# Optimization experiments

Measured on AMD Instinct MI355X. Metric: run time of the kernel, lower is better.

Reference implementation:

```python
import jax, jax.numpy as jnp
import numpy as np

B, S, D, H, DK, F = 4, 2048, 1024, 16, 64, 4096


def layer_norm(x, g, b, eps=1e-5):
    mu = jnp.mean(x, axis=-1, keepdims=True)
    var = jnp.var(x, axis=-1, keepdims=True)
    return (x - mu) * jax.lax.rsqrt(var + eps) * g + b


def setup_inputs() -> dict:
    key = jax.random.key(0)
    ks = jax.random.split(key, 16)
    s = 0.02
    return {
        "src": jax.random.normal(ks[0], (B, S, D), jnp.float32),
        # per-head q/k/v projections stacked over heads: (H, D, DK)
        "Wq": jax.random.normal(ks[1], (H, D, DK), jnp.float32) * s,
        "bq": jnp.zeros((H, DK), jnp.float32),
        "Wk": jax.random.normal(ks[2], (H, D, DK), jnp.float32) * s,
        "bk": jnp.zeros((H, DK), jnp.float32),
        "Wv": jax.random.normal(ks[3], (H, D, DK), jnp.float32) * s,
        "bv": jnp.zeros((H, DK), jnp.float32),
        "Wo": jax.random.normal(ks[4], (H * DK, D), jnp.float32) * s,
        "bo": jnp.zeros((D,), jnp.float32),
        "ln1_g": jnp.ones((D,), jnp.float32),
        "ln1_b": jnp.zeros((D,), jnp.float32),
        "W1": jax.random.normal(ks[5], (D, F), jnp.float32) * s,
        "b1": jnp.zeros((F,), jnp.float32),
        "W2": jax.random.normal(ks[6], (F, D), jnp.float32) * s,
        "b2": jnp.zeros((D,), jnp.float32),
        "ln2_g": jnp.ones((D,), jnp.float32),
        "ln2_b": jnp.zeros((D,), jnp.float32),
    }


def reference(src, Wq, bq, Wk, bk, Wv, bv, Wo, bo, ln1_g, ln1_b, W1, b1, W2, b2, ln2_g, ln2_b):
    # --- multi-head attention (all heads batched via einsum) ---
    q = jnp.einsum("bsd,hdk->bhsk", src, Wq) + bq[None, :, None, :]
    k = jnp.einsum("bsd,hdk->bhsk", src, Wk) + bk[None, :, None, :]
    v = jnp.einsum("bsd,hdk->bhsk", src, Wv) + bv[None, :, None, :]
    scale = jnp.sqrt(jnp.asarray(DK, q.dtype))
    scores = jnp.einsum("bhqk,bhsk->bhqs", q, k) / scale  # [B,H,S,S]
    p = jax.nn.softmax(scores, axis=-1)
    ctx = jnp.einsum("bhqs,bhsk->bhqk", p, v)             # [B,H,S,DK]
    ctx = ctx.transpose(0, 2, 1, 3).reshape(src.shape[0], src.shape[1], H * DK)
    attn_out = ctx @ Wo + bo
    x = layer_norm(src + attn_out, ln1_g, ln1_b)
    # --- feed-forward ---
    ff = jax.nn.relu(x @ W1 + b1) @ W2 + b2
    return layer_norm(x + ff, ln2_g, ln2_b)
```

## Files before the change

### kernel.cpp

```cpp
#include <hip/hip_runtime.h>
#include <hip/hip_bf16.h>
#include <cstddef>
#include <cstdint>

typedef __bf16 bf16;
typedef __bf16 bf16x4 __attribute__((ext_vector_type(4)));
typedef __bf16 bf16x8 __attribute__((ext_vector_type(8)));
typedef float f32x4 __attribute__((ext_vector_type(4)));
typedef float f32x16 __attribute__((ext_vector_type(16)));
typedef unsigned int u32x4 __attribute__((ext_vector_type(4)));

#define GLD_LDS16(g, l) __builtin_amdgcn_global_load_lds( \
    (const __attribute__((address_space(1))) void*)(g),   \
    (__attribute__((address_space(3))) void*)(l), 16, 0, 0)

#define SBAR __builtin_amdgcn_s_barrier()
#define SCHED0 __builtin_amdgcn_sched_barrier(0)
#define VMW(n) asm volatile("s_waitcnt vmcnt(" #n ")" ::: "memory")

static __device__ inline unsigned int cvtpk(float lo, float hi) {
  unsigned int r;
  asm("v_cvt_pk_bf16_f32 %0, %1, %2" : "=v"(r) : "v"(lo), "v"(hi));
  return r;
}
static __device__ inline void plswap(unsigned int& a, unsigned int& b) {
  asm("v_permlane32_swap_b32 %0, %1" : "+v"(a), "+v"(b));
}
static __device__ inline float fexp2(float x) {
#if __has_builtin(__builtin_amdgcn_exp2f)
  return __builtin_amdgcn_exp2f(x);
#else
  float r; asm("v_exp_f32 %0, %1" : "=v"(r) : "v"(x)); return r;
#endif
}
static __device__ inline float tsum16(const float* e) {
  float s0 = e[0] + e[1], s1 = e[2] + e[3], s2 = e[4] + e[5], s3 = e[6] + e[7];
  float s4 = e[8] + e[9], s5 = e[10] + e[11], s6 = e[12] + e[13], s7 = e[14] + e[15];
  return ((s0 + s1) + (s2 + s3)) + ((s4 + s5) + (s6 + s7));
}

__global__ void __launch_bounds__(256)
k_cast(const float* __restrict__ in, bf16* __restrict__ out) {
  int gid = blockIdx.x * 256 + threadIdx.x;
  f32x4 a = ((const f32x4*)in)[gid * 2];
  f32x4 b = ((const f32x4*)in)[gid * 2 + 1];
  bf16x8 o;
#pragma unroll
  for (int i = 0; i < 4; ++i) { o[i] = (bf16)a[i]; o[i + 4] = (bf16)b[i]; }
  ((bf16x8*)out)[gid] = o;
}

__global__ void __launch_bounds__(256)
k_transpose_t(const float* __restrict__ in, bf16* __restrict__ out, int R, int C) {
  __shared__ float tile[64][68];
  const int nct = C >> 6;
  const int bc = blockIdx.x % nct, br = blockIdx.x / nct;
  const int r0 = br << 6, c0 = bc << 6;
  const int t = threadIdx.x;
  const int tr = t >> 4, tc4 = (t & 15) << 2;
#pragma unroll
  for (int i = 0; i < 4; ++i)
    *(f32x4*)&tile[i * 16 + tr][tc4] =
        *(const f32x4*)&in[(size_t)(r0 + i * 16 + tr) * C + c0 + tc4];
  __syncthreads();
  const int c = t >> 2, rch = (t & 3) << 4;
  bf16 ob[16];
#pragma unroll
  for (int j = 0; j < 16; ++j) ob[j] = (bf16)tile[rch + j][c];
  bf16* dst = out + (size_t)(c0 + c) * R + r0 + rch;
  *(bf16x8*)&dst[0] = *(bf16x8*)&ob[0];
  *(bf16x8*)&dst[8] = *(bf16x8*)&ob[8];
}

__global__ void __launch_bounds__(256)
k_reorder_qkv_t(const float* __restrict__ Wq, const float* __restrict__ Wk,
                const float* __restrict__ Wv, bf16* __restrict__ WqkvT) {
  __shared__ float tile[64][68];
  const int bid = blockIdx.x;
  const int sub = bid >> 4, tl = bid & 15;
  const int proj = sub >> 4, h = sub & 15;
  const float* W = (proj == 0) ? Wq : (proj == 1) ? Wk : Wv;
  const float* src = W + (size_t)h * 65536;
  const int r0 = tl << 6;
  const int t = threadIdx.x, tr = t >> 4, tc4 = (t & 15) << 2;
#pragma unroll
  for (int i = 0; i < 4; ++i)
    *(f32x4*)&tile[i * 16 + tr][tc4] =
        *(const f32x4*)&src[(size_t)(r0 + i * 16 + tr) * 64 + tc4];
  __syncthreads();
  const int c = t >> 2, rch = (t & 3) << 4;
  bf16 ob[16];
#pragma unroll
  for (int j = 0; j < 16; ++j) ob[j] = (bf16)tile[rch + j][c];
  bf16* dst = WqkvT + ((size_t)(proj * 1024 + h * 64 + c)) * 1024 + r0 + rch;
  *(bf16x8*)&dst[0] = *(bf16x8*)&ob[0];
  *(bf16x8*)&dst[8] = *(bf16x8*)&ob[8];
}

__global__ void __launch_bounds__(256)
k_bias_qkv(const float* __restrict__ bq, const float* __restrict__ bk,
           const float* __restrict__ bv, float* __restrict__ bqkv) {
  int n = blockIdx.x * 256 + threadIdx.x;
  int proj = n >> 10, wi = n & 1023;
  const float* bb = (proj == 0) ? bq : (proj == 1) ? bk : bv;
  bqkv[n] = bb[wi];
}

template <int MODE, int NREP>
__global__ void __launch_bounds__(512, 1)
k_gemm4(const bf16* __restrict__ A, const bf16* __restrict__ Bt,
        const float* __restrict__ bias, void* __restrict__ outp,
        int M, int N, int K,
        bf16* __restrict__ qb, bf16* __restrict__ kb, bf16* __restrict__ vb) {
  constexpr int BN = 128 * NREP;
  constexpr int BROWS = 64 * NREP;
  __shared__ __align__(16) bf16 Asl[4][8192];
  __shared__ __align__(16) bf16 Bsl[4][BROWS * 64];

  const int tid = threadIdx.x;
  const int lane = tid & 63, wave = tid >> 6;
  const int l16 = lane & 15, lq = lane >> 4;
  const int qwm = wave >> 2, qwn = wave & 3;

  const int mtiles = M >> 8;
  const int wg = blockIdx.x;
  const int tile_m = (wg % mtiles) << 8;
  const int tile_n = (wg / mtiles) * BN;

  const bf16* Abase = A + (size_t)tile_m * K;
  const bf16* Bbase = Bt + (size_t)tile_n * K;

  const int crow = tid >> 3;
  const int ccol = ((tid & 7) ^ (crow & 7)) << 3;

  auto stageA = [&](int T, int h, int slot) {
    const bf16* s_ = Abase + (size_t)(h * 128 + crow) * K + T * 64 + ccol;
    GLD_LDS16(s_, &Asl[slot][tid * 8]);
    GLD_LDS16(s_ + (size_t)64 * K, &Asl[slot][tid * 8 + 4096]);
  };
  auto stageB = [&](int T, int h, int slot) {
    const bf16* s_ = Bbase + (size_t)(h * BROWS + crow) * K + T * 64 + ccol;
    GLD_LDS16(s_, &Bsl[slot][tid * 8]);
    if (NREP == 2) GLD_LDS16(s_ + (size_t)64 * K, &Bsl[slot][tid * 8 + 4096]);
  };

  const int xk = l16 & 7;
  const int swz0 = (lq ^ xk) * 16;
  const int swz1 = ((4 | lq) ^ xk) * 16;
  const int arow_b = (qwm * 64 + l16) * 128;
  const int brow_b = (qwn * 16 * NREP + l16) * 128;

  bf16x8 af[4][2];
  bf16x8 bb[2][NREP][2];
  f32x4 acc[2][2][4][NREP] = {};

  auto dsA = [&](int slot) {
    const char* Ab = (const char*)&Asl[slot][0] + arow_b;
#pragma unroll
    for (int mi = 0; mi < 4; ++mi) {
      af[mi][0] = *(const bf16x8*)(Ab + mi * 2048 + swz0);
      af[mi][1] = *(const bf16x8*)(Ab + mi * 2048 + swz1);
    }
  };
  auto dsB2 = [&](int slot0, int slot1) {
    const char* B0 = (const char*)&Bsl[slot0][0] + brow_b;
    const char* B1 = (const char*)&Bsl[slot1][0] + brow_b;
#pragma unroll
    for (int ni = 0; ni < NREP; ++ni) {
      bb[0][ni][0] = *(const bf16x8*)(B0 + ni * 2048 + swz0);
      bb[0][ni][1] = *(const bf16x8*)(B0 + ni * 2048 + swz1);
      bb[1][ni][0] = *(const bf16x8*)(B1 + ni * 2048 + swz0);
      bb[1][ni][1] = *(const bf16x8*)(B1 + ni * 2048 + swz1);
    }
  };
  auto MF2 = [&](int mh) {
    __builtin_amdgcn_s_setprio(1);
#pragma unroll
    for (int nh = 0; nh < 2; ++nh)
#pragma unroll
      for (int mi = 0; mi < 4; ++mi)
#pragma unroll
        for (int ni = 0; ni < NREP; ++ni)
#pragma unroll
          for (int p = 0; p < 2; ++p)
            acc[mh][nh][mi][ni] = __builtin_amdgcn_mfma_f32_16x16x32_bf16(
                af[mi][p], bb[nh][ni][p], acc[mh][nh][mi][ni], 0, 0, 0);
    __builtin_amdgcn_s_setprio(0);
  };

  const int NT = K >> 6;
  const int NI = NT >> 1;

  stageA(0, 0, 0); stageA(0, 1, 1); stageB(0, 0, 0); stageB(0, 1, 1);
  stageA(1, 0, 2); stageB(1, 0, 2); stageB(1, 1, 3);
  SCHED0;
  if (NREP == 2) { VMW(6); } else { VMW(4); }
  SBAR;

  for (int i = 0; i < NI; ++i) {
    const int t2 = 2 * i + 2, t3 = 2 * i + 3;
    const bool tv = (t2 < NT);
    dsA(0); dsB2(0, 1);
    stageA(2 * i + 1, 1, 3);
    SCHED0;
    if (NREP == 2) { VMW(10); } else { VMW(7); }
    SBAR; MF2(0); SBAR;
    dsA(1);
    if (tv) { stageA(t2, 0, 0); stageB(t2, 0, 0); }
    SCHED0;
    if (!tv) { VMW(2); }
    else if (NREP == 2) { VMW(6); } else { VMW(5); }
    SBAR; MF2(1); SBAR;
    dsA(2); dsB2(2, 3);
    if (tv) { stageA(t2, 1, 1); stageB(t2, 1, 1); }
    SCHED0;
    if (!tv) { VMW(0); }
    else if (NREP == 2) { VMW(8); } else { VMW(6); }
    SBAR; MF2(0); SBAR;
    dsA(3);
    if (tv) {
      stageA(t3, 0, 2); stageB(t3, 0, 2); stageB(t3, 1, 3);
      SCHED0;
      if (NREP == 2) { VMW(6); } else { VMW(4); }
    }
    SBAR; MF2(1); SBAR;
  }

#pragma unroll
  for (int mh = 0; mh < 2; ++mh)
#pragma unroll
    for (int nh = 0; nh < 2; ++nh)
#pragma unroll
      for (int mi = 0; mi < 4; ++mi)
#pragma unroll
        for (int ni = 0; ni < NREP; ++ni) {
          const int gn = tile_n + nh * (BN / 2) + qwn * 16 * NREP + ni * 16 + l16;
          const float bv = bias[gn];
          f32x4 v = acc[mh][nh][mi][ni];
          const int gm0 = tile_m + mh * 128 + qwm * 64 + mi * 16 + lq * 4;
          if (MODE == 0) {
            int proj = gn >> 10, wi = gn & 1023;
            int h = wi >> 6, dk = wi & 63;
            int b = gm0 >> 11, sdx = gm0 & 2047;
            size_t bhs = (size_t)((b << 4) + h);
            if (proj == 0) {
#pragma unroll
              for (int i2 = 0; i2 < 4; ++i2)
                qb[(bhs * 2048 + sdx + i2) * 64 + dk] = (bf16)((v[i2] + bv) * 0.18033688f);
            } else if (proj == 1) {
#pragma unroll
              for (int i2 = 0; i2 < 4; ++i2)
                kb[(bhs * 2048 + sdx + i2) * 64 + dk] = (bf16)(v[i2] + bv);
            } else {
              bf16x4 pk;
#pragma unroll
              for (int i2 = 0; i2 < 4; ++i2) pk[i2] = (bf16)(v[i2] + bv);
              *(bf16x4*)&vb[(bhs * 64 + dk) * 2048 + sdx] = pk;
            }
          } else if (MODE == 1) {
#pragma unroll
            for (int i2 = 0; i2 < 4; ++i2)
              ((bf16*)outp)[(size_t)(gm0 + i2) * N + gn] = (bf16)(v[i2] + bv);
          } else {
#pragma unroll
            for (int i2 = 0; i2 < 4; ++i2)
              ((bf16*)outp)[(size_t)(gm0 + i2) * N + gn] = (bf16)fmaxf(v[i2] + bv, 0.f);
          }
        }
}

__global__ void __launch_bounds__(256, 2)
k_attn(const bf16* __restrict__ qb, const bf16* __restrict__ kb,
       const bf16* __restrict__ vb, bf16* __restrict__ ctx) {
  __shared__ __align__(16) bf16 KsL[3][4096];
  __shared__ __align__(16) bf16 VsL[3][4096];

  const int bid = blockIdx.x;
  const int wg = (bid & 7) * 64 + (bid >> 3);
  const int bh = wg >> 3, qt = wg & 7;

  const bf16* Qp  = qb + (size_t)bh * 131072 + (size_t)qt * 16384;
  const bf16* Kbh = kb + (size_t)bh * 131072;
  const bf16* Vbh = vb + (size_t)bh * 131072;

  const int tid = threadIdx.x, wave = tid >> 6, lane = tid & 63;
  const int l31 = lane & 31, hi = lane >> 5;

  bf16x8 qfA[4], qfB[4];
  {
    const bf16* qra = Qp + (size_t)(wave * 64 + l31) * 64 + hi * 8;
    const bf16* qrb = qra + 32 * 64;
#pragma unroll
    for (int kd = 0; kd < 4; ++kd) {
      qfA[kd] = *(const bf16x8*)(qra + kd * 16);
      qfB[kd] = *(const bf16x8*)(qrb + kd * 16);
    }
  }

  const int c0 = tid, c1 = tid + 256;
  const int sw0 = ((c0 ^ (c0 >> 3)) & 7) * 8, rw0 = c0 >> 3;
  const int sw1 = ((c1 ^ (c1 >> 3)) & 7) * 8, rw1 = c1 >> 3;
  const int kof0 = rw0 * 64 + sw0, kof1 = rw1 * 64 + sw1;
  const int vof0 = rw0 * 2048 + sw0, vof1 = rw1 * 2048 + sw1;

  const int xr = (hi << 4) ^ ((l31 & 7) << 4);
  const int rb = l31 * 128 + xr;

  f32x16 oA[2] = {}, oB[2] = {};
  float lA = 0.f, lB = 0.f;

#define STAGE_KV(buf, s0)                                             \
  do {                                                                \
    GLD_LDS16(Kbh + (size_t)(s0) * 64 + kof0, &KsL[buf][c0 * 8]);     \
    GLD_LDS16(Kbh + (size_t)(s0) * 64 + kof1, &KsL[buf][c1 * 8]);     \
    GLD_LDS16(Vbh + (s0) + vof0, &VsL[buf][c0 * 8]);                  \
    GLD_LDS16(Vbh + (s0) + vof1, &VsL[buf][c1 * 8]);                  \
  } while (0)

  STAGE_KV(0, 0);
  STAGE_KV(1, 64);

  int cur = 0;
  for (int kt = 0; kt < 32; ++kt) {
    SCHED0;
    if (kt == 31) { VMW(0); }
    else          { VMW(4); }
    __builtin_amdgcn_s_barrier();
    SCHED0;

    if (kt < 30) {
      int nx = cur + 2; if (nx >= 3) nx -= 3;
      STAGE_KV(nx, (kt + 2) * 64);
    }

    const char* Kc = (const char*)&KsL[cur][0];
    const char* Vc = (const char*)&VsL[cur][0];

    bf16x8 paA[4], paB[4];
#pragma unroll
    for (int st = 0; st < 2; ++st) {
      f32x16 sA = {}, sB = {};
      __builtin_amdgcn_s_setprio(1);
#pragma unroll
      for (int kd = 0; kd < 4; ++kd) {
        bf16x8 a = *(const bf16x8*)(Kc + st * 4096 + (rb ^ (kd << 5)));
        sA = __builtin_amdgcn_mfma_f32_32x32x16_bf16(a, qfA[kd], sA, 0, 0, 0);
        sB = __builtin_amdgcn_mfma_f32_32x32x16_bf16(a, qfB[kd], sB, 0, 0, 0);
      }
      __builtin_amdgcn_s_setprio(0);

      float eA[16], eB[16];
#pragma unroll
      for (int i = 0; i < 16; ++i) {
        eA[i] = fexp2(sA[i]);
        eB[i] = fexp2(sB[i]);
      }
      lA += tsum16(eA);
      lB += tsum16(eB);
      unsigned int qdA[4][2], qdB[4][2];
#pragma unroll
      for (int g = 0; g < 4; ++g)
#pragma unroll
        for (int w = 0; w < 2; ++w) {
          qdA[g][w] = cvtpk(eA[g * 4 + w * 2], eA[g * 4 + w * 2 + 1]);
          qdB[g][w] = cvtpk(eB[g * 4 + w * 2], eB[g * 4 + w * 2 + 1]);
        }
#pragma unroll
      for (int a2 = 0; a2 < 2; ++a2) {
        unsigned int x0 = qdA[2 * a2][0], y0 = qdA[2 * a2 + 1][0];
        unsigned int x1 = qdA[2 * a2][1], y1 = qdA[2 * a2 + 1][1];
        plswap(x0, y0); plswap(x1, y1);
        u32x4 fA = {x0, x1, y0, y1};
        paA[st * 2 + a2] = __builtin_bit_cast(bf16x8, fA);
        unsigned int u0 = qdB[2 * a2][0], v0 = qdB[2 * a2 + 1][0];
        unsigned int u1 = qdB[2 * a2][1], v1 = qdB[2 * a2 + 1][1];
        plswap(u0, v0); plswap(u1, v1);
        u32x4 fB = {u0, u1, v0, v1};
        paB[st * 2 + a2] = __builtin_bit_cast(bf16x8, fB);
      }
    }

    __builtin_amdgcn_s_setprio(1);
#pragma unroll
    for (int nd = 0; nd < 2; ++nd)
#pragma unroll
      for (int ks = 0; ks < 4; ++ks) {
        bf16x8 vf = *(const bf16x8*)(Vc + nd * 4096 + (rb ^ (ks << 5)));
        oA[nd] = __builtin_amdgcn_mfma_f32_32x32x16_bf16(paA[ks], vf, oA[nd], 0, 0, 0);
        oB[nd] = __builtin_amdgcn_mfma_f32_32x32x16_bf16(paB[ks], vf, oB[nd], 0, 0, 0);
      }
    __builtin_amdgcn_s_setprio(0);

    if (++cur == 3) cur = 0;
  }
#undef STAGE_KV

  const float ltA = lA + __shfl_xor(lA, 32);
  const float ltB = lB + __shfl_xor(lB, 32);
  const float ivA = 1.f / ltA;
  const float ivB = 1.f / ltB;

  const int b = bh >> 4, h = bh & 15;
  const size_t rowbase = (size_t)(b * 2048 + qt * 256 + wave * 64);
#pragma unroll
  for (int r = 0; r < 16; ++r) {
    const int qr = (r & 3) + 8 * (r >> 2) + 4 * hi;
    const float dA = __shfl(ivA, qr);
    const float dB = __shfl(ivB, qr);
#pragma unroll
    for (int nd = 0; nd < 2; ++nd) {
      const int dk = nd * 32 + l31;
      ctx[(rowbase + qr) * 1024 + h * 64 + dk]      = (bf16)(oA[nd][r] * dA);
      ctx[(rowbase + 32 + qr) * 1024 + h * 64 + dk] = (bf16)(oB[nd][r] * dB);
    }
  }
}

template <typename RT, typename DT, typename OT>
__global__ void __launch_bounds__(256)
k_ln(const RT* __restrict__ resid, const DT* __restrict__ delta,
     const float* __restrict__ g, const float* __restrict__ bta,
     OT* __restrict__ out) {
  const int row = blockIdx.x, tid = threadIdx.x;
  const int wave = tid >> 6, lane = tid & 63;
  __shared__ float rs_[4], rs2_[4];
  const RT* r = resid + (size_t)row * 1024;
  const DT* d = delta + (size_t)row * 1024;
  OT* o = out + (size_t)row * 1024;
  float x[4], s = 0.f, s2 = 0.f;
#pragma unroll
  for (int j = 0; j < 4; ++j) {
    int idx = tid + j * 256;
    float v = (float)r[idx] + (float)d[idx];
    x[j] = v; s += v; s2 += v * v;
  }
#pragma unroll
  for (int m = 32; m >= 1; m >>= 1) { s += __shfl_xor(s, m); s2 += __shfl_xor(s2, m); }
  if (lane == 0) { rs_[wave] = s; rs2_[wave] = s2; }
  __syncthreads();
  float ts = rs_[0] + rs_[1] + rs_[2] + rs_[3];
  float ts2 = rs2_[0] + rs2_[1] + rs2_[2] + rs2_[3];
  float mean = ts * (1.f / 1024.f);
  float var = ts2 * (1.f / 1024.f) - mean * mean;
  float rstd = rsqrtf(var + 1e-5f);
#pragma unroll
  for (int j = 0; j < 4; ++j) {
    int idx = tid + j * 256;
    o[idx] = (OT)((x[j] - mean) * rstd * g[idx] + bta[idx]);
  }
}

extern "C" void kernel_launch(void* const* d_in, const int* in_sizes, int n_in,
                              void* d_out, int out_size, void* d_ws, size_t ws_size,
                              hipStream_t stream) {
  const float* src  = (const float*)d_in[0];
  const float* Wq   = (const float*)d_in[1];
  const float* bq   = (const float*)d_in[2];
  const float* Wk   = (const float*)d_in[3];
  const float* bk   = (const float*)d_in[4];
  const float* Wv   = (const float*)d_in[5];
  const float* bv   = (const float*)d_in[6];
  const float* Wo   = (const float*)d_in[7];
  const float* bo   = (const float*)d_in[8];
  const float* ln1g = (const float*)d_in[9];
  const float* ln1b = (const float*)d_in[10];
  const float* W1   = (const float*)d_in[11];
  const float* b1   = (const float*)d_in[12];
  const float* W2   = (const float*)d_in[13];
  const float* b2   = (const float*)d_in[14];
  const float* ln2g = (const float*)d_in[15];
  const float* ln2b = (const float*)d_in[16];

  char* p = (char*)d_ws;
  bf16*  WqkvT = (bf16*)p;  p += (size_t)3072 * 1024 * 2;
  float* bqkv  = (float*)p; p += 16384;
  bf16*  WoT   = (bf16*)p;  p += (size_t)1024 * 1024 * 2;
  bf16*  W1T   = (bf16*)p;  p += (size_t)4096 * 1024 * 2;
  bf16*  W2T   = (bf16*)p;  p += (size_t)1024 * 4096 * 2;
  bf16*  srcb  = (bf16*)p;  p += (size_t)8388608 * 2;
  bf16*  qbuf  = (bf16*)p;  p += (size_t)8388608 * 2;
  bf16*  kbuf  = (bf16*)p;  p += (size_t)8388608 * 2;
  bf16*  vbuf  = (bf16*)p;  p += (size_t)8388608 * 2;
  bf16*  ctx   = (bf16*)p;  p += (size_t)8388608 * 2;
  bf16*  x1    = (bf16*)p;  p += (size_t)8388608 * 2;
  bf16*  ff1   = (bf16*)p;  p += (size_t)8192 * 4096 * 2;
  bf16*  tmp   = qbuf;

  k_cast<<<4096, 256, 0, stream>>>(src, srcb);
  k_reorder_qkv_t<<<768, 256, 0, stream>>>(Wq, Wk, Wv, WqkvT);
  k_bias_qkv<<<12, 256, 0, stream>>>(bq, bk, bv, bqkv);
  k_transpose_t<<<256, 256, 0, stream>>>(Wo, WoT, 1024, 1024);
  k_transpose_t<<<1024, 256, 0, stream>>>(W1, W1T, 1024, 4096);
  k_transpose_t<<<1024, 256, 0, stream>>>(W2, W2T, 4096, 1024);

  k_gemm4<0, 1><<<768, 512, 0, stream>>>(srcb, WqkvT, bqkv, nullptr,
                                         8192, 3072, 1024, qbuf, kbuf, vbuf);
  k_attn<<<512, 256, 0, stream>>>(qbuf, kbuf, vbuf, ctx);
  k_gemm4<1, 1><<<256, 512, 0, stream>>>(ctx, WoT, bo, tmp,
                                         8192, 1024, 1024, nullptr, nullptr, nullptr);
  k_ln<float, bf16, bf16><<<8192, 256, 0, stream>>>(src, tmp, ln1g, ln1b, x1);
  k_gemm4<2, 2><<<512, 512, 0, stream>>>(x1, W1T, b1, ff1,
                                         8192, 4096, 1024, nullptr, nullptr, nullptr);
  k_gemm4<1, 1><<<256, 512, 0, stream>>>(ff1, W2T, b2, tmp,
                                         8192, 1024, 4096, nullptr, nullptr, nullptr);
  k_ln<bf16, bf16, float><<<8192, 256, 0, stream>>>(x1, tmp, ln2g, ln2b, (float*)d_out);
}
```

Baseline: 493.3 us.

## Add 128x256-tile triple-buffered GEMM kernel for QKV, Wo and W2 projections

Introduces k_gemmS, a GEMM with 128-row by 256-column tiles, a 3-slot LDS ring filled via global_load_lds, and MFMA work split into two halves with raised wave priority. The QKV projection, the output projection and the second FFN GEMM switch to it; the W1 GEMM stays on k_gemm4. The aim is a better A/B reuse ratio for these shapes and a simpler, lower-latency load/compute pipeline than the old 4-stage kernel. The risk is lower overlap from shallower buffering, and higher register pressure from 16 accumulators plus fragment arrays. The QKV scatter epilogue moves out of k_gemm4, which now keeps only modes 1 and 2.

```diff
diff --git a/kernel.cpp b/kernel.cpp
--- a/kernel.cpp
+++ b/kernel.cpp
@@ -104,6 +104,143 @@
   int proj = n >> 10, wi = n & 1023;
   const float* bb = (proj == 0) ? bq : (proj == 1) ? bk : bv;
   bqkv[n] = bb[wi];
+}
+
+template <int MODE>
+__global__ void __launch_bounds__(512, 1)
+k_gemmS(const bf16* __restrict__ A, const bf16* __restrict__ Bt,
+        const float* __restrict__ bias, void* __restrict__ outp,
+        int M, int N, int K,
+        bf16* __restrict__ qb, bf16* __restrict__ kb, bf16* __restrict__ vb) {
+  __shared__ __align__(16) bf16 Asl[3][8192];
+  __shared__ __align__(16) bf16 Bsl[3][16384];
+
+  const int tid = threadIdx.x;
+  const int lane = tid & 63, wave = tid >> 6;
+  const int l16 = lane & 15, lq = lane >> 4;
+  const int qwm = wave >> 2, qwn = wave & 3;
+
+  const int mtiles = M >> 7;
+  const int wg = blockIdx.x;
+  const int tile_m = (wg % mtiles) << 7;
+  const int tile_n = (wg / mtiles) << 8;
+
+  const bf16* Abase = A + (size_t)tile_m * K;
+  const bf16* Bbase = Bt + (size_t)tile_n * K;
+
+  const int crow = tid >> 3;
+  const int ccol = ((tid & 7) ^ (crow & 7)) << 3;
+
+  auto STAGE = [&](int T, int slot) {
+    const bf16* a_ = Abase + (size_t)crow * K + T * 64 + ccol;
+    GLD_LDS16(a_, &Asl[slot][tid * 8]);
+    GLD_LDS16(a_ + (size_t)64 * K, &Asl[slot][tid * 8 + 4096]);
+    const bf16* b_ = Bbase + (size_t)crow * K + T * 64 + ccol;
+    GLD_LDS16(b_, &Bsl[slot][tid * 8]);
+    GLD_LDS16(b_ + (size_t)64 * K, &Bsl[slot][tid * 8 + 4096]);
+    GLD_LDS16(b_ + (size_t)128 * K, &Bsl[slot][tid * 8 + 8192]);
+    GLD_LDS16(b_ + (size_t)192 * K, &Bsl[slot][tid * 8 + 12288]);
+  };
+
+  const int xk = l16 & 7;
+  const int swz0 = (lq ^ xk) * 16;
+  const int swz1 = ((4 | lq) ^ xk) * 16;
+  const int arow_b = (qwm * 64 + l16) * 128;
+  const int brow_b = (qwn * 64 + l16) * 128;
+
+  f32x4 acc[4][4] = {};
+
+  const int NT = K >> 6;
+  STAGE(0, 0); STAGE(1, 1);
+
+  for (int t = 0; t < NT; ++t) {
+    const int slot = t % 3;
+    if (t + 2 < NT) STAGE(t + 2, (t + 2) % 3);
+    SCHED0;
+    if (t + 2 < NT) { VMW(12); }
+    else if (t + 1 < NT) { VMW(6); }
+    else { VMW(0); }
+    SBAR;
+    SCHED0;
+
+    const char* Ab = (const char*)&Asl[slot][0] + arow_b;
+    const char* Bb = (const char*)&Bsl[slot][0] + brow_b;
+    bf16x8 af[4][2], bfr[4][2];
+#pragma unroll
+    for (int mi = 0; mi < 4; ++mi) {
+      af[mi][0] = *(const bf16x8*)(Ab + mi * 2048 + swz0);
+      af[mi][1] = *(const bf16x8*)(Ab + mi * 2048 + swz1);
+    }
+#pragma unroll
+    for (int ni = 0; ni < 2; ++ni) {
+      bfr[ni][0] = *(const bf16x8*)(Bb + ni * 2048 + swz0);
+      bfr[ni][1] = *(const bf16x8*)(Bb + ni * 2048 + swz1);
+    }
+    __builtin_amdgcn_s_setprio(1);
+#pragma unroll
+    for (int mi = 0; mi < 4; ++mi)
+#pragma unroll
+      for (int ni = 0; ni < 2; ++ni)
+#pragma unroll
+        for (int p = 0; p < 2; ++p)
+          acc[mi][ni] = __builtin_amdgcn_mfma_f32_16x16x32_bf16(
+              af[mi][p], bfr[ni][p], acc[mi][ni], 0, 0, 0);
+    __builtin_amdgcn_s_setprio(0);
+#pragma unroll
+    for (int ni = 2; ni < 4; ++ni) {
+      bfr[ni][0] = *(const bf16x8*)(Bb + ni * 2048 + swz0);
+      bfr[ni][1] = *(const bf16x8*)(Bb + ni * 2048 + swz1);
+    }
+    __builtin_amdgcn_s_setprio(1);
+#pragma unroll
+    for (int mi = 0; mi < 4; ++mi)
+#pragma unroll
+      for (int ni = 2; ni < 4; ++ni)
+#pragma unroll
+        for (int p = 0; p < 2; ++p)
+          acc[mi][ni] = __builtin_amdgcn_mfma_f32_16x16x32_bf16(
+              af[mi][p], bfr[ni][p], acc[mi][ni], 0, 0, 0);
+    __builtin_amdgcn_s_setprio(0);
+    SBAR;
+  }
+
+#pragma unroll
+  for (int mi = 0; mi < 4; ++mi)
+#pragma unroll
+    for (int ni = 0; ni < 4; ++ni) {
+      const int gn = tile_n + qwn * 64 + ni * 16 + l16;
+      const float bv = bias[gn];
+      f32x4 v = acc[mi][ni];
+      const int gm0 = tile_m + qwm * 64 + mi * 16 + lq * 4;
+      if (MODE == 0) {
+        int proj = gn >> 10, wi = gn & 1023;
+        int h = wi >> 6, dk = wi & 63;
+        int b = gm0 >> 11, sdx = gm0 & 2047;
+        size_t bhs = (size_t)((b << 4) + h);
+        if (proj == 0) {
+#pragma unroll
+          for (int i2 = 0; i2 < 4; ++i2)
+            qb[(bhs * 2048 + sdx + i2) * 64 + dk] = (bf16)((v[i2] + bv) * 0.18033688f);
+        } else if (proj == 1) {
+#pragma unroll
+          for (int i2 = 0; i2 < 4; ++i2)
+            kb[(bhs * 2048 + sdx + i2) * 64 + dk] = (bf16)(v[i2] + bv);
+        } else {
+          bf16x4 pk;
+#pragma unroll
+          for (int i2 = 0; i2 < 4; ++i2) pk[i2] = (bf16)(v[i2] + bv);
+          *(bf16x4*)&vb[(bhs * 64 + dk) * 2048 + sdx] = pk;
+        }
+      } else if (MODE == 1) {
+#pragma unroll
+        for (int i2 = 0; i2 < 4; ++i2)
+          ((bf16*)outp)[(size_t)(gm0 + i2) * N + gn] = (bf16)(v[i2] + bv);
+      } else {
+#pragma unroll
+        for (int i2 = 0; i2 < 4; ++i2)
+          ((bf16*)outp)[(size_t)(gm0 + i2) * N + gn] = (bf16)fmaxf(v[i2] + bv, 0.f);
+      }
+    }
 }
 
 template <int MODE, int NREP>
@@ -238,26 +375,7 @@
           const float bv = bias[gn];
           f32x4 v = acc[mh][nh][mi][ni];
           const int gm0 = tile_m + mh * 128 + qwm * 64 + mi * 16 + lq * 4;
-          if (MODE == 0) {
-            int proj = gn >> 10, wi = gn & 1023;
-            int h = wi >> 6, dk = wi & 63;
-            int b = gm0 >> 11, sdx = gm0 & 2047;
-            size_t bhs = (size_t)((b << 4) + h);
-            if (proj == 0) {
-#pragma unroll
-              for (int i2 = 0; i2 < 4; ++i2)
-                qb[(bhs * 2048 + sdx + i2) * 64 + dk] = (bf16)((v[i2] + bv) * 0.18033688f);
-            } else if (proj == 1) {
-#pragma unroll
-              for (int i2 = 0; i2 < 4; ++i2)
-                kb[(bhs * 2048 + sdx + i2) * 64 + dk] = (bf16)(v[i2] + bv);
-            } else {
-              bf16x4 pk;
-#pragma unroll
-              for (int i2 = 0; i2 < 4; ++i2) pk[i2] = (bf16)(v[i2] + bv);
-              *(bf16x4*)&vb[(bhs * 64 + dk) * 2048 + sdx] = pk;
-            }
-          } else if (MODE == 1) {
+          if (MODE == 1) {
 #pragma unroll
             for (int i2 = 0; i2 < 4; ++i2)
               ((bf16*)outp)[(size_t)(gm0 + i2) * N + gn] = (bf16)(v[i2] + bv);
@@ -493,15 +611,15 @@
   k_transpose_t<<<1024, 256, 0, stream>>>(W1, W1T, 1024, 4096);
   k_transpose_t<<<1024, 256, 0, stream>>>(W2, W2T, 4096, 1024);
 
-  k_gemm4<0, 1><<<768, 512, 0, stream>>>(srcb, WqkvT, bqkv, nullptr,
-                                         8192, 3072, 1024, qbuf, kbuf, vbuf);
+  k_gemmS<0><<<768, 512, 0, stream>>>(srcb, WqkvT, bqkv, nullptr,
+                                      8192, 3072, 1024, qbuf, kbuf, vbuf);
   k_attn<<<512, 256, 0, stream>>>(qbuf, kbuf, vbuf, ctx);
-  k_gemm4<1, 1><<<256, 512, 0, stream>>>(ctx, WoT, bo, tmp,
-                                         8192, 1024, 1024, nullptr, nullptr, nullptr);
+  k_gemmS<1><<<256, 512, 0, stream>>>(ctx, WoT, bo, tmp,
+                                      8192, 1024, 1024, nullptr, nullptr, nullptr);
   k_ln<float, bf16, bf16><<<8192, 256, 0, stream>>>(src, tmp, ln1g, ln1b, x1);
   k_gemm4<2, 2><<<512, 512, 0, stream>>>(x1, W1T, b1, ff1,
                                          8192, 4096, 1024, nullptr, nullptr, nullptr);
-  k_gemm4<1, 1><<<256, 512, 0, stream>>>(ff1, W2T, b2, tmp,
-                                         8192, 1024, 4096, nullptr, nullptr, nullptr);
+  k_gemmS<1><<<256, 512, 0, stream>>>(ff1, W2T, b2, tmp,
+                                      8192, 1024, 4096, nullptr, nullptr, nullptr);
   k_ln<bf16, bf16, float><<<8192, 256, 0, stream>>>(x1, tmp, ln2g, ln2b, (float*)d_out);
 }
```

Measured after the change: 504.6 us. +2.3%, slower.

## Split-K the FFN down-projection with wider tiles and fuse partial reduction into LayerNorm

Applied to the files above, without the earlier changes.

The W2 GEMM now uses 256x256 tiles (NREP=2) with a 2-way split over K, writing fp32 partial sums into the free workspace. A new LayerNorm kernel adds both partials, the bias and the residual before normalising. The aim is more data reuse per block while keeping 256 blocks in flight, at the cost of extra fp32 partial traffic. Separately, the GEMM pipeline drops two vmcnt waits and lowers the others, which reduces stalls in every GEMM but risks reading LDS before loads land.

```diff
diff --git a/kernel.cpp b/kernel.cpp
--- a/kernel.cpp
+++ b/kernel.cpp
@@ -110,7 +110,7 @@
 __global__ void __launch_bounds__(512, 1)
 k_gemm4(const bf16* __restrict__ A, const bf16* __restrict__ Bt,
         const float* __restrict__ bias, void* __restrict__ outp,
-        int M, int N, int K,
+        int M, int N, int K, int klen, int splitk,
         bf16* __restrict__ qb, bf16* __restrict__ kb, bf16* __restrict__ vb) {
   constexpr int BN = 128 * NREP;
   constexpr int BROWS = 64 * NREP;
@@ -122,13 +122,16 @@
   const int l16 = lane & 15, lq = lane >> 4;
   const int qwm = wave >> 2, qwn = wave & 3;
 
+  const int tiles = gridDim.x / splitk;
+  const int twg = blockIdx.x % tiles;
+  const int sk = blockIdx.x / tiles;
+  const int k0 = sk * klen;
   const int mtiles = M >> 8;
-  const int wg = blockIdx.x;
-  const int tile_m = (wg % mtiles) << 8;
-  const int tile_n = (wg / mtiles) * BN;
-
-  const bf16* Abase = A + (size_t)tile_m * K;
-  const bf16* Bbase = Bt + (size_t)tile_n * K;
+  const int tile_m = (twg % mtiles) << 8;
+  const int tile_n = (twg / mtiles) * BN;
+
+  const bf16* Abase = A + (size_t)tile_m * K + k0;
+  const bf16* Bbase = Bt + (size_t)tile_n * K + k0;
 
   const int crow = tid >> 3;
   const int ccol = ((tid & 7) ^ (crow & 7)) << 3;
@@ -188,7 +191,7 @@
     __builtin_amdgcn_s_setprio(0);
   };
 
-  const int NT = K >> 6;
+  const int NT = klen >> 6;
   const int NI = NT >> 1;
 
   stageA(0, 0, 0); stageA(0, 1, 1); stageB(0, 0, 0); stageB(0, 1, 1);
@@ -202,20 +205,15 @@
     const bool tv = (t2 < NT);
     dsA(0); dsB2(0, 1);
     stageA(2 * i + 1, 1, 3);
-    SCHED0;
-    if (NREP == 2) { VMW(10); } else { VMW(7); }
     SBAR; MF2(0); SBAR;
     dsA(1);
     if (tv) { stageA(t2, 0, 0); stageB(t2, 0, 0); }
     SCHED0;
-    if (!tv) { VMW(2); }
-    else if (NREP == 2) { VMW(6); } else { VMW(5); }
+    if (!tv) { VMW(0); }
+    else if (NREP == 2) { VMW(4); } else { VMW(3); }
     SBAR; MF2(1); SBAR;
     dsA(2); dsB2(2, 3);
     if (tv) { stageA(t2, 1, 1); stageB(t2, 1, 1); }
-    SCHED0;
-    if (!tv) { VMW(0); }
-    else if (NREP == 2) { VMW(8); } else { VMW(6); }
     SBAR; MF2(0); SBAR;
     dsA(3);
     if (tv) {
@@ -226,6 +224,7 @@
     SBAR; MF2(1); SBAR;
   }
 
+  float* psplit = (MODE == 3) ? ((float*)outp + (size_t)sk * M * N) : nullptr;
 #pragma unroll
   for (int mh = 0; mh < 2; ++mh)
 #pragma unroll
@@ -235,7 +234,7 @@
 #pragma unroll
         for (int ni = 0; ni < NREP; ++ni) {
           const int gn = tile_n + nh * (BN / 2) + qwn * 16 * NREP + ni * 16 + l16;
-          const float bv = bias[gn];
+          const float bv = (MODE == 3) ? 0.f : bias[gn];
           f32x4 v = acc[mh][nh][mi][ni];
           const int gm0 = tile_m + mh * 128 + qwm * 64 + mi * 16 + lq * 4;
           if (MODE == 0) {
@@ -261,10 +260,14 @@
 #pragma unroll
             for (int i2 = 0; i2 < 4; ++i2)
               ((bf16*)outp)[(size_t)(gm0 + i2) * N + gn] = (bf16)(v[i2] + bv);
-          } else {
+          } else if (MODE == 2) {
 #pragma unroll
             for (int i2 = 0; i2 < 4; ++i2)
               ((bf16*)outp)[(size_t)(gm0 + i2) * N + gn] = (bf16)fmaxf(v[i2] + bv, 0.f);
+          } else {
+#pragma unroll
+            for (int i2 = 0; i2 < 4; ++i2)
+              psplit[(size_t)(gm0 + i2) * N + gn] = v[i2];
           }
         }
 }
@@ -447,6 +450,41 @@
   for (int j = 0; j < 4; ++j) {
     int idx = tid + j * 256;
     o[idx] = (OT)((x[j] - mean) * rstd * g[idx] + bta[idx]);
+  }
+}
+
+__global__ void __launch_bounds__(256)
+k_ln_sk(const bf16* __restrict__ x1r, const float* __restrict__ p0,
+        const float* __restrict__ p1, const float* __restrict__ bias,
+        const float* __restrict__ g, const float* __restrict__ bta,
+        float* __restrict__ out) {
+  const int row = blockIdx.x, tid = threadIdx.x;
+  const int wave = tid >> 6, lane = tid & 63;
+  __shared__ float rs_[4], rs2_[4];
+  const bf16* r = x1r + (size_t)row * 1024;
+  const float* a = p0 + (size_t)row * 1024;
+  const float* b = p1 + (size_t)row * 1024;
+  float* o = out + (size_t)row * 1024;
+  float x[4], s = 0.f, s2 = 0.f;
+#pragma unroll
+  for (int j = 0; j < 4; ++j) {
+    int idx = tid + j * 256;
+    float v = (float)r[idx] + a[idx] + b[idx] + bias[idx];
+    x[j] = v; s += v; s2 += v * v;
+  }
+#pragma unroll
+  for (int m = 32; m >= 1; m >>= 1) { s += __shfl_xor(s, m); s2 += __shfl_xor(s2, m); }
+  if (lane == 0) { rs_[wave] = s; rs2_[wave] = s2; }
+  __syncthreads();
+  float ts = rs_[0] + rs_[1] + rs_[2] + rs_[3];
+  float ts2 = rs2_[0] + rs2_[1] + rs2_[2] + rs2_[3];
+  float mean = ts * (1.f / 1024.f);
+  float var = ts2 * (1.f / 1024.f) - mean * mean;
+  float rstd = rsqrtf(var + 1e-5f);
+#pragma unroll
+  for (int j = 0; j < 4; ++j) {
+    int idx = tid + j * 256;
+    o[idx] = (x[j] - mean) * rstd * g[idx] + bta[idx];
   }
 }
 
@@ -485,6 +523,7 @@
   bf16*  x1    = (bf16*)p;  p += (size_t)8388608 * 2;
   bf16*  ff1   = (bf16*)p;  p += (size_t)8192 * 4096 * 2;
   bf16*  tmp   = qbuf;
+  float* pk0   = (float*)srcb;
 
   k_cast<<<4096, 256, 0, stream>>>(src, srcb);
   k_reorder_qkv_t<<<768, 256, 0, stream>>>(Wq, Wk, Wv, WqkvT);
@@ -494,14 +533,15 @@
   k_transpose_t<<<1024, 256, 0, stream>>>(W2, W2T, 4096, 1024);
 
   k_gemm4<0, 1><<<768, 512, 0, stream>>>(srcb, WqkvT, bqkv, nullptr,
-                                         8192, 3072, 1024, qbuf, kbuf, vbuf);
+                                         8192, 3072, 1024, 1024, 1, qbuf, kbuf, vbuf);
   k_attn<<<512, 256, 0, stream>>>(qbuf, kbuf, vbuf, ctx);
   k_gemm4<1, 1><<<256, 512, 0, stream>>>(ctx, WoT, bo, tmp,
-                                         8192, 1024, 1024, nullptr, nullptr, nullptr);
+                                         8192, 1024, 1024, 1024, 1, nullptr, nullptr, nullptr);
   k_ln<float, bf16, bf16><<<8192, 256, 0, stream>>>(src, tmp, ln1g, ln1b, x1);
   k_gemm4<2, 2><<<512, 512, 0, stream>>>(x1, W1T, b1, ff1,
-                                         8192, 4096, 1024, nullptr, nullptr, nullptr);
-  k_gemm4<1, 1><<<256, 512, 0, stream>>>(ff1, W2T, b2, tmp,
-                                         8192, 1024, 4096, nullptr, nullptr, nullptr);
-  k_ln<bf16, bf16, float><<<8192, 256, 0, stream>>>(x1, tmp, ln2g, ln2b, (float*)d_out);
-}
+                                         8192, 4096, 1024, 1024, 1, nullptr, nullptr, nullptr);
+  k_gemm4<3, 2><<<256, 512, 0, stream>>>(ff1, W2T, nullptr, pk0,
+                                         8192, 1024, 4096, 2048, 2, nullptr, nullptr, nullptr);
+  k_ln_sk<<<8192, 256, 0, stream>>>(x1, pk0, pk0 + (size_t)8192 * 1024, b2,
+                                    ln2g, ln2b, (float*)d_out);
+}
```

Result: faster. 482.2 us (-2.2%).
